# Kernel optimization log

Hardware: AMD Instinct MI355X
Metric: run time of the kernel (lower is better)

## Reference

```python
import jax, jax.numpy as jnp
import numpy as np

DIM = 512
NUM_HEADS = 16
WIN = (7, 7)
SIZE = WIN[0] * WIN[1]  # 49
B = 2048   # total windows
NW = 4     # windows per image (mask groups)


def _relative_position_index():
    coords_h = np.arange(WIN[0])
    coords_w = np.arange(WIN[1])
    coords = np.stack(np.meshgrid(coords_h, coords_w, indexing='ij'))  # [2,Wh,Ww]
    flat = coords.reshape(2, -1)                                       # [2,S]
    rel = flat[:, :, None] - flat[:, None, :]                          # [2,S,S]
    rel = rel.transpose(1, 2, 0)                                       # [S,S,2]
    rel[:, :, 0] += WIN[0] - 1
    rel[:, :, 1] += WIN[1] - 1
    rel[:, :, 0] *= 2 * WIN[1] - 1
    return rel.sum(-1).astype(np.int32)                                # [S,S]


def setup_inputs() -> dict:
    key = jax.random.key(0)
    ks = jax.random.split(key, 8)
    num_bias = (2 * WIN[0] - 1) * (2 * WIN[1] - 1)  # 169
    sd = 1.0 / np.sqrt(DIM)
    return {
        'x': jax.random.normal(ks[0], (B, SIZE, DIM), dtype=jnp.float32),
        'mask': jax.random.normal(ks[1], (NW, SIZE, SIZE), dtype=jnp.float32),
        'w_qkv': jax.random.normal(ks[2], (DIM, 3 * DIM), dtype=jnp.float32) * sd,
        'b_qkv': jnp.zeros((3 * DIM,), dtype=jnp.float32),
        'w_proj': jax.random.normal(ks[3], (DIM, DIM), dtype=jnp.float32) * sd,
        'b_proj': jnp.zeros((DIM,), dtype=jnp.float32),
        'bias_table': jax.random.normal(ks[4], (num_bias, NUM_HEADS), dtype=jnp.float32) * 0.02,
        'rel_idx': jnp.asarray(_relative_position_index()),
    }


def reference(x, mask, w_qkv, b_qkv, w_proj, b_proj, bias_table, rel_idx):
    b, s, c = x.shape
    h = NUM_HEADS
    hd = c // h
    scale = hd ** (-0.5)
    # qkv projection -> [3, B, H, S, hd]
    qkv = (x @ w_qkv + b_qkv).reshape(b, s, 3, h, hd).transpose(2, 0, 3, 1, 4)
    q, k, v = qkv[0] * scale, qkv[1], qkv[2]
    attn = jnp.einsum('bhqd,bhkd->bhqk', q, k)                 # [B,H,S,S]
    # gathered relative position bias -> [H,S,S]
    bias = bias_table[rel_idx.reshape(-1)].reshape(s, s, h).transpose(2, 0, 1)
    attn = attn + bias[None]
    nw = mask.shape[0]
    attn = attn.reshape(b // nw, nw, h, s, s) + mask[None, :, None]
    attn = jax.nn.softmax(attn.reshape(b, h, s, s), axis=-1)
    out = jnp.einsum('bhqk,bhkd->bhqd', attn, v)               # [B,H,S,hd]
    out = out.transpose(0, 2, 1, 3).reshape(b, s, c)
    return out @ w_proj + b_proj
```

## Files before the change

### kernel.cpp

```cpp
#include <hip/hip_runtime.h>
#include <hip/hip_bf16.h>
#include <stdint.h>

typedef float  floatx4 __attribute__((ext_vector_type(4)));
typedef short  short8  __attribute__((ext_vector_type(8)));
typedef unsigned short u16;

#define DIM 512
#define NH 16
#define HD 32
#define WS 49
#define NBW 2048
#define NWIN 4
#define M_TOTAL (NBW*WS)
#define N_QKV (3*DIM)

__device__ __forceinline__ u16 f2bf(float f) {
    uint32_t u = __float_as_uint(f);
    u += 0x7FFFu + ((u >> 16) & 1u);
    return (u16)(u >> 16);
}

__device__ __forceinline__ void load_lds16(const u16* g, u16* l) {
    __builtin_amdgcn_global_load_lds(
        (const __attribute__((address_space(1))) unsigned int*)g,
        (__attribute__((address_space(3))) unsigned int*)l, 16, 0, 0);
}

__global__ void cast_x_kernel(const float* __restrict__ in, u16* __restrict__ out, int n4) {
    int i = blockIdx.x * blockDim.x + threadIdx.x;
    if (i >= n4) return;
    const float4 v = ((const float4*)in)[i];
    ushort4 o;
    o.x = f2bf(v.x); o.y = f2bf(v.y); o.z = f2bf(v.z); o.w = f2bf(v.w);
    ((ushort4*)out)[i] = o;
}

__global__ void transpose_cast_kernel(const float* __restrict__ in, u16* __restrict__ out,
                                      int N, int total) {
    int idx = blockIdx.x * blockDim.x + threadIdx.x;
    if (idx >= total) return;
    int k = idx & (DIM - 1);
    int n = idx >> 9;
    out[idx] = f2bf(in[k * N + n]);
}

__global__ void build_comb_kernel(const float* __restrict__ bias_table, const int* __restrict__ rel_idx,
                                  const float* __restrict__ mask, float* __restrict__ comb) {
    int idx = blockIdx.x * blockDim.x + threadIdx.x;
    if (idx >= NWIN * NH * 64 * 64) return;
    int j = idx & 63, i = (idx >> 6) & 63, h = (idx >> 12) & 15, g = idx >> 16;
    float v = -1e30f;
    if (i < WS && j < WS)
        v = bias_table[rel_idx[i * WS + j] * NH + h] + mask[(g * WS + i) * WS + j];
    comb[idx] = v;
}

template<bool OUT_BF16>
__global__ __launch_bounds__(256, 2) void gemm_bt_kernel(
    const u16* __restrict__ A, const u16* __restrict__ Bt,
    const float* __restrict__ bias, void* __restrict__ out, int N, int K)
{
    __shared__ __align__(16) u16 sA[128 * 32];
    __shared__ __align__(16) u16 sB[128 * 32];
    const int tid  = threadIdx.x;
    const int lane = tid & 63;
    const int wave = tid >> 6;
    const long m0 = (long)blockIdx.y * 128;
    const long n0 = (long)blockIdx.x * 128;
    const int rr = lane & 15;
    const int qk = (lane >> 4) * 8;
    const int wm = (wave >> 1) * 64;
    const int wn = (wave & 1) * 64;

    floatx4 acc[4][4];
    const floatx4 z4 = {0.f, 0.f, 0.f, 0.f};
#pragma unroll
    for (int mi = 0; mi < 4; ++mi)
#pragma unroll
        for (int ni = 0; ni < 4; ++ni) acc[mi][ni] = z4;

    const int row0 = tid >> 2;
    const int kc0  = (tid & 3) * 8;
    const u16* gA0 = A  + (m0 + row0) * K + kc0;
    const u16* gA1 = A  + (m0 + row0 + 64) * K + kc0;
    const u16* gB0 = Bt + (n0 + row0) * K + kc0;
    const u16* gB1 = Bt + (n0 + row0 + 64) * K + kc0;
    u16* lA0 = sA + tid * 8;
    u16* lA1 = sA + (tid + 256) * 8;
    u16* lB0 = sB + tid * 8;
    u16* lB1 = sB + (tid + 256) * 8;

    for (int k0 = 0; k0 < K; k0 += 32) {
        load_lds16(gA0 + k0, lA0);
        load_lds16(gA1 + k0, lA1);
        load_lds16(gB0 + k0, lB0);
        load_lds16(gB1 + k0, lB1);
        __syncthreads();
        short8 af[4], bfr[4];
#pragma unroll
        for (int mi = 0; mi < 4; ++mi)
            af[mi] = *(const short8*)(sA + (wm + mi * 16 + rr) * 32 + qk);
#pragma unroll
        for (int ni = 0; ni < 4; ++ni)
            bfr[ni] = *(const short8*)(sB + (wn + ni * 16 + rr) * 32 + qk);
#pragma unroll
        for (int mi = 0; mi < 4; ++mi)
#pragma unroll
            for (int ni = 0; ni < 4; ++ni)
                acc[mi][ni] = __builtin_amdgcn_mfma_f32_16x16x32_bf16(af[mi], bfr[ni], acc[mi][ni], 0, 0, 0);
        __syncthreads();
    }

#pragma unroll
    for (int mi = 0; mi < 4; ++mi) {
#pragma unroll
        for (int r = 0; r < 4; ++r) {
            const long m = m0 + wm + mi * 16 + (lane >> 4) * 4 + r;
#pragma unroll
            for (int ni = 0; ni < 4; ++ni) {
                const long n = n0 + wn + ni * 16 + rr;
                float v = acc[mi][ni][r] + bias[n];
                if (OUT_BF16) ((u16*)out)[m * N + n] = f2bf(v);
                else          ((float*)out)[m * N + n] = v;
            }
        }
    }
}

__global__ __launch_bounds__(64) void attn_kernel(
    const u16* __restrict__ qkv, const float* __restrict__ comb,
    u16* __restrict__ attn_out)
{
    const int bh = blockIdx.x;
    const int b = bh >> 4, h = bh & 15;
    const int l = threadIdx.x;
    const int rr = l & 15;
    const int qk = (l >> 4) * 8;

    __shared__ __align__(16) u16 qk_s[2 * 64 * 32];
    __shared__ __align__(16) u16 vT_s[32 * 64];
    __shared__ float rsum[64];
    u16* q_s = qk_s;
    u16* k_s = qk_s + 64 * 32;
    u16* p_s = qk_s;

    const u16* qg = qkv + (long)b * WS * N_QKV + h * HD;
    const u16* kg = qg + DIM;
    const u16* vg = qg + 2 * DIM;

    for (int i = l; i < 32 * 64 / 2; i += 64) ((unsigned int*)vT_s)[i] = 0u;
    __syncthreads();
    for (int c = l; c < 256; c += 64) {
        const int row = c >> 2, kc8 = (c & 3) * 8;
        uint4 zq = {0, 0, 0, 0}, zk = {0, 0, 0, 0};
        if (row < WS) {
            zq = *(const uint4*)(qg + (long)row * N_QKV + kc8);
            zk = *(const uint4*)(kg + (long)row * N_QKV + kc8);
        }
        *(uint4*)(q_s + c * 8) = zq;
        *(uint4*)(k_s + c * 8) = zk;
    }
    for (int t = l; t < WS * HD; t += 64) {
        const int row = t >> 5, d = t & 31;
        vT_s[d * 64 + row] = vg[(long)row * N_QKV + d];
    }
    __syncthreads();

    short8 af[4], bfr[4];
#pragma unroll
    for (int mi = 0; mi < 4; ++mi) af[mi] = *(const short8*)(q_s + (mi * 16 + rr) * 32 + qk);
#pragma unroll
    for (int ni = 0; ni < 4; ++ni) bfr[ni] = *(const short8*)(k_s + (ni * 16 + rr) * 32 + qk);
    __syncthreads();

    floatx4 sc[4][4];
    const floatx4 z4 = {0.f, 0.f, 0.f, 0.f};
#pragma unroll
    for (int mi = 0; mi < 4; ++mi)
#pragma unroll
        for (int ni = 0; ni < 4; ++ni)
            sc[mi][ni] = __builtin_amdgcn_mfma_f32_16x16x32_bf16(af[mi], bfr[ni], z4, 0, 0, 0);

    const float* cb = comb + (long)((b & (NWIN - 1)) * NH + h) * 4096;
    const float scale = 0.17677669529663689f;
#pragma unroll
    for (int mi = 0; mi < 4; ++mi) {
#pragma unroll
        for (int r = 0; r < 4; ++r) {
            const int i = mi * 16 + (l >> 4) * 4 + r;
            float s0 = sc[mi][0][r] * scale + cb[i * 64 +  0 + rr];
            float s1 = sc[mi][1][r] * scale + cb[i * 64 + 16 + rr];
            float s2 = sc[mi][2][r] * scale + cb[i * 64 + 32 + rr];
            float s3 = sc[mi][3][r] * scale + cb[i * 64 + 48 + rr];
            float mx = fmaxf(fmaxf(s0, s1), fmaxf(s2, s3));
#pragma unroll
            for (int off = 1; off < 16; off <<= 1) mx = fmaxf(mx, __shfl_xor(mx, off, 64));
            float e0 = __expf(s0 - mx), e1 = __expf(s1 - mx);
            float e2 = __expf(s2 - mx), e3 = __expf(s3 - mx);
            float sm = e0 + e1 + e2 + e3;
#pragma unroll
            for (int off = 1; off < 16; off <<= 1) sm += __shfl_xor(sm, off, 64);
            p_s[i * 64 +  0 + rr] = f2bf(e0);
            p_s[i * 64 + 16 + rr] = f2bf(e1);
            p_s[i * 64 + 32 + rr] = f2bf(e2);
            p_s[i * 64 + 48 + rr] = f2bf(e3);
            if (rr == 0) rsum[i] = sm;
        }
    }
    __syncthreads();

    floatx4 oacc[4][2];
#pragma unroll
    for (int mi = 0; mi < 4; ++mi) { oacc[mi][0] = z4; oacc[mi][1] = z4; }
#pragma unroll
    for (int kk = 0; kk < 2; ++kk) {
        short8 pf[4], vf[2];
#pragma unroll
        for (int mi = 0; mi < 4; ++mi)
            pf[mi] = *(const short8*)(p_s + (mi * 16 + rr) * 64 + kk * 32 + qk);
#pragma unroll
        for (int ni = 0; ni < 2; ++ni)
            vf[ni] = *(const short8*)(vT_s + (ni * 16 + rr) * 64 + kk * 32 + qk);
#pragma unroll
        for (int mi = 0; mi < 4; ++mi)
#pragma unroll
            for (int ni = 0; ni < 2; ++ni)
                oacc[mi][ni] = __builtin_amdgcn_mfma_f32_16x16x32_bf16(pf[mi], vf[ni], oacc[mi][ni], 0, 0, 0);
    }

#pragma unroll
    for (int mi = 0; mi < 4; ++mi) {
#pragma unroll
        for (int r = 0; r < 4; ++r) {
            const int i = mi * 16 + (l >> 4) * 4 + r;
            if (i < WS) {
                const float inv = 1.0f / rsum[i];
                u16* op = attn_out + ((long)(b * WS + i)) * DIM + h * HD;
                op[rr]      = f2bf(oacc[mi][0][r] * inv);
                op[16 + rr] = f2bf(oacc[mi][1][r] * inv);
            }
        }
    }
}

extern "C" void kernel_launch(void* const* d_in, const int* in_sizes, int n_in,
                              void* d_out, int out_size, void* d_ws, size_t ws_size,
                              hipStream_t stream)
{
    const float* x          = (const float*)d_in[0];
    const float* mask       = (const float*)d_in[1];
    const float* w_qkv      = (const float*)d_in[2];
    const float* b_qkv      = (const float*)d_in[3];
    const float* w_proj     = (const float*)d_in[4];
    const float* b_proj     = (const float*)d_in[5];
    const float* bias_table = (const float*)d_in[6];
    const int*   rel_idx    = (const int*)d_in[7];
    float* out = (float*)d_out;

    char* ws = (char*)d_ws;
    u16* x_bf   = (u16*)ws;  ws += (size_t)M_TOTAL * DIM * 2;
    u16* wqkvT  = (u16*)ws;  ws += (size_t)N_QKV * DIM * 2;
    u16* wprojT = (u16*)ws;  ws += (size_t)DIM * DIM * 2;
    float* comb = (float*)ws; ws += (size_t)NWIN * NH * 64 * 64 * 4;
    u16* qkv    = (u16*)ws;  ws += (size_t)M_TOTAL * N_QKV * 2;
    u16* attn_o = x_bf;

    const int n4 = M_TOTAL * DIM / 4;
    cast_x_kernel<<<(n4 + 255) / 256, 256, 0, stream>>>(x, x_bf, n4);
    transpose_cast_kernel<<<(N_QKV * DIM + 255) / 256, 256, 0, stream>>>(w_qkv, wqkvT, N_QKV, N_QKV * DIM);
    transpose_cast_kernel<<<(DIM * DIM + 255) / 256, 256, 0, stream>>>(w_proj, wprojT, DIM, DIM * DIM);
    build_comb_kernel<<<(NWIN * NH * 64 * 64 + 255) / 256, 256, 0, stream>>>(bias_table, rel_idx, mask, comb);

    gemm_bt_kernel<true><<<dim3(N_QKV / 128, M_TOTAL / 128), 256, 0, stream>>>(
        x_bf, wqkvT, b_qkv, qkv, N_QKV, DIM);

    attn_kernel<<<NBW * NH, 64, 0, stream>>>(qkv, comb, attn_o);

    gemm_bt_kernel<false><<<dim3(DIM / 128, M_TOTAL / 128), 256, 0, stream>>>(
        attn_o, wprojT, b_proj, out, DIM, DIM);
}
```

Measured before the change: 941.7 us.

## Load Q/K/V MFMA fragments directly from global and swizzle P in LDS

Result: faster. 905.7 us (-3.8%).

```diff
diff --git a/kernel.cpp b/kernel.cpp
--- a/kernel.cpp
+++ b/kernel.cpp
@@ -128,7 +128,7 @@
     }
 }
 
-__global__ __launch_bounds__(64) void attn_kernel(
+__global__ __launch_bounds__(64, 4) void attn_kernel(
     const u16* __restrict__ qkv, const float* __restrict__ comb,
     u16* __restrict__ attn_out)
 {
@@ -136,43 +136,27 @@
     const int b = bh >> 4, h = bh & 15;
     const int l = threadIdx.x;
     const int rr = l & 15;
-    const int qk = (l >> 4) * 8;
-
-    __shared__ __align__(16) u16 qk_s[2 * 64 * 32];
-    __shared__ __align__(16) u16 vT_s[32 * 64];
-    __shared__ float rsum[64];
-    u16* q_s = qk_s;
-    u16* k_s = qk_s + 64 * 32;
-    u16* p_s = qk_s;
+    const int q4 = l >> 4;
+    const int qk = q4 * 8;
+
+    __shared__ __align__(16) u16 p_s[64 * 64];
 
     const u16* qg = qkv + (long)b * WS * N_QKV + h * HD;
     const u16* kg = qg + DIM;
     const u16* vg = qg + 2 * DIM;
 
-    for (int i = l; i < 32 * 64 / 2; i += 64) ((unsigned int*)vT_s)[i] = 0u;
-    __syncthreads();
-    for (int c = l; c < 256; c += 64) {
-        const int row = c >> 2, kc8 = (c & 3) * 8;
-        uint4 zq = {0, 0, 0, 0}, zk = {0, 0, 0, 0};
-        if (row < WS) {
-            zq = *(const uint4*)(qg + (long)row * N_QKV + kc8);
-            zk = *(const uint4*)(kg + (long)row * N_QKV + kc8);
-        }
-        *(uint4*)(q_s + c * 8) = zq;
-        *(uint4*)(k_s + c * 8) = zk;
-    }
-    for (int t = l; t < WS * HD; t += 64) {
-        const int row = t >> 5, d = t & 31;
-        vT_s[d * 64 + row] = vg[(long)row * N_QKV + d];
-    }
-    __syncthreads();
-
     short8 af[4], bfr[4];
-#pragma unroll
-    for (int mi = 0; mi < 4; ++mi) af[mi] = *(const short8*)(q_s + (mi * 16 + rr) * 32 + qk);
-#pragma unroll
-    for (int ni = 0; ni < 4; ++ni) bfr[ni] = *(const short8*)(k_s + (ni * 16 + rr) * 32 + qk);
-    __syncthreads();
+    const short8 z8 = {0, 0, 0, 0, 0, 0, 0, 0};
+#pragma unroll
+    for (int mi = 0; mi < 4; ++mi) {
+        const int row = mi * 16 + rr;
+        af[mi] = (row < WS) ? *(const short8*)(qg + (long)row * N_QKV + qk) : z8;
+    }
+#pragma unroll
+    for (int ni = 0; ni < 4; ++ni) {
+        const int row = ni * 16 + rr;
+        bfr[ni] = (row < WS) ? *(const short8*)(kg + (long)row * N_QKV + qk) : z8;
+    }
 
     floatx4 sc[4][4];
     const floatx4 z4 = {0.f, 0.f, 0.f, 0.f};
@@ -182,13 +166,29 @@
         for (int ni = 0; ni < 4; ++ni)
             sc[mi][ni] = __builtin_amdgcn_mfma_f32_16x16x32_bf16(af[mi], bfr[ni], z4, 0, 0, 0);
 
+    short8 vf[2][2];
+#pragma unroll
+    for (int kk = 0; kk < 2; ++kk)
+#pragma unroll
+        for (int ni = 0; ni < 2; ++ni) {
+            short8 t = z8;
+            const int d = ni * 16 + rr;
+#pragma unroll
+            for (int j = 0; j < 8; ++j) {
+                const int s = kk * 32 + qk + j;
+                if (s < WS) t[j] = (short)vg[(long)s * N_QKV + d];
+            }
+            vf[kk][ni] = t;
+        }
+
     const float* cb = comb + (long)((b & (NWIN - 1)) * NH + h) * 4096;
     const float scale = 0.17677669529663689f;
+    float inv_s[4][4];
 #pragma unroll
     for (int mi = 0; mi < 4; ++mi) {
 #pragma unroll
         for (int r = 0; r < 4; ++r) {
-            const int i = mi * 16 + (l >> 4) * 4 + r;
+            const int i = mi * 16 + q4 * 4 + r;
             float s0 = sc[mi][0][r] * scale + cb[i * 64 +  0 + rr];
             float s1 = sc[mi][1][r] * scale + cb[i * 64 + 16 + rr];
             float s2 = sc[mi][2][r] * scale + cb[i * 64 + 32 + rr];
@@ -201,11 +201,14 @@
             float sm = e0 + e1 + e2 + e3;
 #pragma unroll
             for (int off = 1; off < 16; off <<= 1) sm += __shfl_xor(sm, off, 64);
-            p_s[i * 64 +  0 + rr] = f2bf(e0);
-            p_s[i * 64 + 16 + rr] = f2bf(e1);
-            p_s[i * 64 + 32 + rr] = f2bf(e2);
-            p_s[i * 64 + 48 + rr] = f2bf(e3);
-            if (rr == 0) rsum[i] = sm;
+            inv_s[mi][r] = 1.0f / sm;
+#pragma unroll
+            for (int c = 0; c < 4; ++c) {
+                const int col = c * 16 + rr;
+                const int blk = (col >> 3) ^ (i & 7);
+                const float ev = (c == 0) ? e0 : (c == 1) ? e1 : (c == 2) ? e2 : e3;
+                p_s[i * 64 + blk * 8 + (col & 7)] = f2bf(ev);
+            }
         }
     }
     __syncthreads();
@@ -215,27 +218,26 @@
     for (int mi = 0; mi < 4; ++mi) { oacc[mi][0] = z4; oacc[mi][1] = z4; }
 #pragma unroll
     for (int kk = 0; kk < 2; ++kk) {
-        short8 pf[4], vf[2];
+        short8 pf[4];
+#pragma unroll
+        for (int mi = 0; mi < 4; ++mi) {
+            const int i2 = mi * 16 + rr;
+            pf[mi] = *(const short8*)(p_s + i2 * 64 + (((4 * kk + q4) ^ (i2 & 7)) * 8));
+        }
 #pragma unroll
         for (int mi = 0; mi < 4; ++mi)
-            pf[mi] = *(const short8*)(p_s + (mi * 16 + rr) * 64 + kk * 32 + qk);
-#pragma unroll
-        for (int ni = 0; ni < 2; ++ni)
-            vf[ni] = *(const short8*)(vT_s + (ni * 16 + rr) * 64 + kk * 32 + qk);
-#pragma unroll
-        for (int mi = 0; mi < 4; ++mi)
 #pragma unroll
             for (int ni = 0; ni < 2; ++ni)
-                oacc[mi][ni] = __builtin_amdgcn_mfma_f32_16x16x32_bf16(pf[mi], vf[ni], oacc[mi][ni], 0, 0, 0);
+                oacc[mi][ni] = __builtin_amdgcn_mfma_f32_16x16x32_bf16(pf[mi], vf[kk][ni], oacc[mi][ni], 0, 0, 0);
     }
 
 #pragma unroll
     for (int mi = 0; mi < 4; ++mi) {
 #pragma unroll
         for (int r = 0; r < 4; ++r) {
-            const int i = mi * 16 + (l >> 4) * 4 + r;
+            const int i = mi * 16 + q4 * 4 + r;
             if (i < WS) {
-                const float inv = 1.0f / rsum[i];
+                const float inv = inv_s[mi][r];
                 u16* op = attn_out + ((long)(b * WS + i)) * DIM + h * HD;
                 op[rr]      = f2bf(oacc[mi][0][r] * inv);
                 op[16 + rr] = f2bf(oacc[mi][1][r] * inv);
```
